# Optimization experiments

Measured on AMD Instinct MI355X. Metric: run time of the kernel, lower is better.

The kernel has to match this reference:

```python
import jax, jax.numpy as jnp
import numpy as np

EPS = 1e-7
MAX_NORM = 10.0  # safe_expmap tangent-norm clamp


def _sinh_div(d):
    # sinh(d)/d, stable at d->0
    ds = jnp.maximum(d, 1e-6)
    return jnp.where(d < 1e-6, 1.0, jnp.sinh(ds) / ds)


def _div_sinh(d):
    # d/sinh(d), stable at d->0
    ds = jnp.maximum(d, 1e-6)
    return jnp.where(d < 1e-6, 1.0, ds / jnp.sinh(ds))


def projx(x):
    # re-project onto hyperboloid: x0 = sqrt(1 + ||x_spatial||^2)
    sp = x[..., 1:]
    x0 = jnp.sqrt(1.0 + jnp.sum(sp * sp, -1, keepdims=True))
    return jnp.concatenate([x0, sp], -1)


def logmap0(x):
    # log map at origin o=(1,0,...,0); tangent has first coord 0
    x0 = jnp.clip(x[..., :1], 1.0 + EPS, None)
    d = jnp.arccosh(x0)
    v_sp = _div_sinh(d) * x[..., 1:]
    return jnp.concatenate([jnp.zeros_like(x0), v_sp], -1)


def safe_expmap0(v):
    # exp map at origin with norm clamping for stability
    sp = v[..., 1:]
    n = jnp.sqrt(jnp.sum(sp * sp, -1, keepdims=True))
    scale = jnp.minimum(1.0, MAX_NORM / jnp.maximum(n, EPS))
    sp = sp * scale
    m = jnp.minimum(n, MAX_NORM)
    return jnp.concatenate([jnp.cosh(m), _sinh_div(m) * sp], -1)


def lorentz_inner(x, y):
    return -x[..., :1] * y[..., :1] + jnp.sum(x[..., 1:] * y[..., 1:], -1, keepdims=True)


def logmap(x, y):
    ip = jnp.clip(lorentz_inner(x, y), None, -(1.0 + EPS))
    d = jnp.arccosh(-ip)
    return _div_sinh(d) * (y + ip * x)


def safe_expmap(x, v):
    # exp map at x with Lorentz-norm clamping
    vv = lorentz_inner(v, v)
    n = jnp.sqrt(jnp.clip(vv, 0.0, None))
    scale = jnp.minimum(1.0, MAX_NORM / jnp.maximum(n, EPS))
    v = v * scale
    m = jnp.minimum(n, MAX_NORM)
    return jnp.cosh(m) * x + _sinh_div(m) * v


def lorentz_linear(x_hyp, W, b):
    # Lorentz -> tangent -> linear -> Lorentz
    y_tan = logmap0(x_hyp) @ W.T + b
    return projx(safe_expmap0(y_tan))


def setup_inputs() -> dict:
    key = jax.random.key(0)
    ks = jax.random.split(key, 8)
    N, D, H = 32768, 256, 1024
    z_sp = 0.5 * jax.random.normal(ks[0], (N, D - 1), dtype=jnp.float32)
    z_h = projx(jnp.concatenate([jnp.zeros((N, 1), jnp.float32), z_sp], -1))
    s = lambda fi, fo: (2.0 / (fi + fo)) ** 0.5
    return {
        "z_h": z_h,
        "w0": s(D, H) * jax.random.normal(ks[1], (H, D), dtype=jnp.float32),
        "b0": jnp.zeros((H,), jnp.float32),
        "w1": s(H, H) * jax.random.normal(ks[2], (H, H), dtype=jnp.float32),
        "b1": jnp.zeros((H,), jnp.float32),
        "w2": s(H, D) * jax.random.normal(ks[3], (D, H), dtype=jnp.float32),
        "b2": jnp.zeros((D,), jnp.float32),
        "alpha": jnp.float32(0.7),
        "step_size": jnp.float32(1.0),
    }


def reference(z_h, w0, b0, w1, b1, w2, b2, alpha, step_size):
    # v_tangent branch: x_previous is None, average_velocity is None
    v_tangent = logmap0(z_h)
    v_hyp = projx(safe_expmap0(v_tangent))

    # LorentzMLP (n_layers=2 -> 3 LorentzLinear layers); dropout is identity (eval)
    x = v_hyp
    for W, b in ((w0, b0), (w1, b1)):
        x = lorentz_linear(x, W, b)
        x = projx(safe_expmap0(logmap0(x)))
    v_transformed_hyp = lorentz_linear(x, w2, b2)

    v_transformed = logmap0(v_transformed_hyp)
    step = jax.nn.sigmoid(step_size)
    v_final = step * v_transformed
    z_update = projx(safe_expmap(z_h, v_final))

    a = jax.nn.sigmoid(alpha)
    tangent_direction = logmap(z_h, z_update)
    scaled_tangent = (1.0 - a) * tangent_direction
    z_next = projx(safe_expmap(z_h, scaled_tangent))
    return (z_next, z_h)
```

## Files before the change

### kernel.cpp

```cpp
#include <hip/hip_runtime.h>
#include <math.h>

#define EPSF 1e-7f
#define MAXN 10.0f

typedef unsigned short ushortT;
typedef __bf16 bf16_8 __attribute__((ext_vector_type(8)));
typedef float f32_4 __attribute__((ext_vector_type(4)));

#define MFMA16 __builtin_amdgcn_mfma_f32_16x16x32_bf16
#define BAR asm volatile("s_barrier" ::: "memory")

__device__ __forceinline__ float sinh_div_f(float d) {
    float ds = fmaxf(d, 1e-6f);
    return (d < 1e-6f) ? 1.0f : sinhf(ds) / ds;
}
__device__ __forceinline__ float div_sinh_f(float d) {
    float ds = fmaxf(d, 1e-6f);
    return (d < 1e-6f) ? 1.0f : ds / sinhf(ds);
}
__device__ __forceinline__ float wred(float v) {
#pragma unroll
    for (int off = 32; off > 0; off >>= 1) v += __shfl_xor(v, off, 64);
    return v;
}
__device__ __forceinline__ float red16(float v) {
    v += __shfl_xor(v, 1, 64); v += __shfl_xor(v, 2, 64);
    v += __shfl_xor(v, 4, 64); v += __shfl_xor(v, 8, 64);
    return v;
}
__device__ __forceinline__ void bsplit(float x, ushortT& h, ushortT& l) {
    unsigned u = __float_as_uint(x);
    unsigned r = (u + 0x7fffu + ((u >> 16) & 1u)) >> 16;
    h = (ushortT)r;
    float lo = x - __uint_as_float(r << 16);
    unsigned ul = __float_as_uint(lo);
    l = (ushortT)((ul + 0x7fffu + ((ul >> 16) & 1u)) >> 16);
}
__device__ __forceinline__ void gload_lds16(const void* g, void* l) {
    __builtin_amdgcn_global_load_lds(
        (const __attribute__((address_space(1))) unsigned int*)g,
        (__attribute__((address_space(3))) unsigned int*)l, 16, 0, 0);
}
__device__ __forceinline__ void split_item(const float* __restrict__ x,
                                           ushortT* __restrict__ hi, ushortT* __restrict__ lo,
                                           int idx) {
    float4 v = reinterpret_cast<const float4*>(x)[idx];
    float f[4] = {v.x, v.y, v.z, v.w};
    ushortT hh[4], ll[4];
#pragma unroll
    for (int e = 0; e < 4; ++e) bsplit(f[e], hh[e], ll[e]);
    reinterpret_cast<ushort4*>(hi)[idx] = ushort4{hh[0], hh[1], hh[2], hh[3]};
    reinterpret_cast<ushort4*>(lo)[idx] = ushort4{ll[0], ll[1], ll[2], ll[3]};
}

__global__ void combo1(const float* __restrict__ z, const float* __restrict__ w0,
                       const float* __restrict__ w1,
                       ushortT* __restrict__ p0h, ushortT* __restrict__ p0l,
                       ushortT* __restrict__ w0h, ushortT* __restrict__ w0l,
                       ushortT* __restrict__ w1h, ushortT* __restrict__ w1l, int N) {
    int b = blockIdx.x, tid = threadIdx.x;
    if (b < 256) {
        split_item(w0, w0h, w0l, b * 256 + tid);
        return;
    }
    if (b < 1280) {
        split_item(w1, w1h, w1l, (b - 256) * 256 + tid);
        return;
    }
    int gw = (b - 1280) * 4 + (tid >> 6);
    int lane = tid & 63;
    if (gw >= N) return;
    float4 zv = reinterpret_cast<const float4*>(z + (size_t)gw * 256)[lane];
    float z0 = __shfl(zv.x, 0, 64);
    float x0 = fmaxf(z0, 1.f + EPSF);
    float d = acoshf(x0);
    float f = div_sinh_f(d);
    float vx = (lane == 0) ? 0.f : zv.x * f;
    float vy = zv.y * f, vz = zv.z * f, vw = zv.w * f;
    float ss = wred(vx * vx + vy * vy + vz * vz + vw * vw);
    float n = sqrtf(ss);
    float s = fminf(1.f, MAXN / fmaxf(n, EPSF));
    float o[4] = {vx * s, vy * s, vz * s, vw * s};
    ushortT hh[4], ll[4];
#pragma unroll
    for (int e = 0; e < 4; ++e) bsplit(o[e], hh[e], ll[e]);
    reinterpret_cast<ushort4*>(p0h + (size_t)gw * 256)[lane] = ushort4{hh[0], hh[1], hh[2], hh[3]};
    reinterpret_cast<ushort4*>(p0l + (size_t)gw * 256)[lane] = ushort4{ll[0], ll[1], ll[2], ll[3]};
}

__global__ void rowscale_kernel(const float* __restrict__ partials, float* __restrict__ scale,
                                int N, int nSlices) {
    int r = blockIdx.x * blockDim.x + threadIdx.x;
    if (r >= N) return;
    float s = 0.f;
    for (int k = 0; k < nSlices; ++k) s += partials[(size_t)k * N + r];
    float n = sqrtf(s);
    scale[r] = fminf(1.f, MAXN / fmaxf(n, EPSF));
}

__global__ void combo2(const float* __restrict__ partials, float* __restrict__ s2,
                       const float* __restrict__ w2,
                       ushortT* __restrict__ w2h, ushortT* __restrict__ w2l, int N) {
    int b = blockIdx.x, tid = threadIdx.x;
    if (b < 128) {
        int r = b * 256 + tid;
        if (r >= N) return;
        float s = 0.f;
        for (int k = 0; k < 16; ++k) s += partials[(size_t)k * N + r];
        float n = sqrtf(s);
        s2[r] = fminf(1.f, MAXN / fmaxf(n, EPSF));
        return;
    }
    split_item(w2, w2h, w2l, (b - 128) * 256 + tid);
}

template<int OUTMODE, int IM>
__global__ __launch_bounds__(512, 2) void gemm_v9(
    const ushortT* __restrict__ Ah_g, const ushortT* __restrict__ Al_g,
    const ushortT* __restrict__ Wh_g, const ushortT* __restrict__ Wl_g,
    const float* __restrict__ bias, const float* __restrict__ scaleA,
    float* __restrict__ outF, ushortT* __restrict__ outH, ushortT* __restrict__ outL,
    float* __restrict__ partials, int K, int M, int nColBlk, int Nrows,
    const float* __restrict__ z_g, const float* __restrict__ alpha_p,
    const float* __restrict__ step_p)
{
    constexpr int BM = IM * 32;
    constexpr int AS = BM * 32;
    constexpr int BS = 256 * 32;
    constexpr int BUF = 2 * AS + 2 * BS;
    constexpr int HM = IM / 2;
    __shared__ __align__(16) ushortT lds[2 * BUF];

    const int tid = threadIdx.x;
    const int wid = tid >> 6, lane = tid & 63;
    const int nwg = gridDim.x;
    const int swz = ((int)blockIdx.x & 7) * (nwg >> 3) + ((int)blockIdx.x >> 3);
    const int rb = swz / nColBlk, cb = swz % nColBlk;
    const int rowBase = rb * BM, colBase = cb * 256;

    const int rl = tid >> 2;
    const int ks = (tid & 3) ^ ((rl >> 1) & 3);
    const int d8 = tid * 8;
    const ushortT* gAh0 = Ah_g + (size_t)(rowBase + rl) * K + ks * 8;
    const ushortT* gAl0 = Al_g + (size_t)(rowBase + rl) * K + ks * 8;
    const ushortT* gAh1 = Ah_g + (size_t)(rowBase + 128 + rl) * K + ks * 8;
    const ushortT* gAl1 = Al_g + (size_t)(rowBase + 128 + rl) * K + ks * 8;
    const ushortT* gBh0 = Wh_g + (size_t)(colBase + rl) * K + ks * 8;
    const ushortT* gBh1 = Wh_g + (size_t)(colBase + 128 + rl) * K + ks * 8;
    const ushortT* gBl0 = Wl_g + (size_t)(colBase + rl) * K + ks * 8;
    const ushortT* gBl1 = Wl_g + (size_t)(colBase + 128 + rl) * K + ks * 8;
#define STG(p, dst, nbo, nk) gload_lds16((p) + (nk), &lds[(nbo) + (dst) + d8])

    const int warpM = wid >> 2, warpN = wid & 3;
    const int frow = lane & 15, fk = lane >> 4;
    const int pslot8 = (fk ^ ((frow >> 1) & 3)) * 8;
    const int aoff = (warpM * (IM * 16) + frow) * 32 + pslot8;
    const int boff = (warpN * 64 + frow) * 32 + pslot8;

    f32_4 acc[IM][4];
#pragma unroll
    for (int i = 0; i < IM; ++i)
#pragma unroll
        for (int j = 0; j < 4; ++j) acc[i][j] = f32_4{0.f, 0.f, 0.f, 0.f};

    STG(gAh0, 0, 0, 0);
    if constexpr (IM == 8) STG(gAh1, 4096, 0, 0);
    STG(gAl0, AS, 0, 0);
    if constexpr (IM == 8) STG(gAl1, AS + 4096, 0, 0);
    STG(gBh0, 2 * AS, 0, 0); STG(gBh1, 2 * AS + 4096, 0, 0);
    STG(gBl0, 2 * AS + BS, 0, 0); STG(gBl1, 2 * AS + BS + 4096, 0, 0);
    asm volatile("s_waitcnt vmcnt(0)" ::: "memory");
    BAR;

    const int nt = K >> 5;
    for (int t = 0; t < nt; ++t) {
        const ushortT* lb = &lds[(t & 1) * BUF];
        const int nbo = ((t & 1) ^ 1) * BUF;
        const int nk = (t + 1) << 5;
        const bool more = (t + 1) < nt;

        if (more) {
            STG(gAh0, 0, nbo, nk);
            if constexpr (IM == 8) STG(gAh1, 4096, nbo, nk);
            STG(gAl0, AS, nbo, nk);
            if constexpr (IM == 8) STG(gAl1, AS + 4096, nbo, nk);
            STG(gBh0, 2 * AS, nbo, nk); STG(gBh1, 2 * AS + 4096, nbo, nk);
            STG(gBl0, 2 * AS + BS, nbo, nk); STG(gBl1, 2 * AS + BS + 4096, nbo, nk);
        }

        bf16_8 ah[IM], bh[4], bl[4], al[IM];
#pragma unroll
        for (int i = 0; i < IM; ++i) ah[i] = *reinterpret_cast<const bf16_8*>(&lb[aoff + i * 512]);
#pragma unroll
        for (int j = 0; j < 4; ++j) bh[j] = *reinterpret_cast<const bf16_8*>(&lb[2 * AS + boff + j * 512]);
        __builtin_amdgcn_s_setprio(1);
#pragma unroll
        for (int i = 0; i < IM; ++i)
#pragma unroll
            for (int j = 0; j < 4; ++j) acc[i][j] = MFMA16(ah[i], bh[j], acc[i][j], 0, 0, 0);
        __builtin_amdgcn_s_setprio(0);

#pragma unroll
        for (int j = 0; j < 4; ++j) bl[j] = *reinterpret_cast<const bf16_8*>(&lb[2 * AS + BS + boff + j * 512]);
        __builtin_amdgcn_s_setprio(1);
#pragma unroll
        for (int i = 0; i < IM; ++i)
#pragma unroll
            for (int j = 0; j < 4; ++j) acc[i][j] = MFMA16(ah[i], bl[j], acc[i][j], 0, 0, 0);
        __builtin_amdgcn_s_setprio(0);

#pragma unroll
        for (int i = 0; i < IM; ++i) al[i] = *reinterpret_cast<const bf16_8*>(&lb[AS + aoff + i * 512]);
        __builtin_amdgcn_s_setprio(1);
#pragma unroll
        for (int i = 0; i < IM; ++i)
#pragma unroll
            for (int j = 0; j < 4; ++j) acc[i][j] = MFMA16(al[i], bh[j], acc[i][j], 0, 0, 0);
        __builtin_amdgcn_s_setprio(0);

        asm volatile("s_waitcnt vmcnt(0)" ::: "memory");
        BAR;
    }
#undef STG

    const int cbase = colBase + warpN * 64 + frow;
    if constexpr (OUTMODE == 0) {
        float bv[4];
#pragma unroll
        for (int j = 0; j < 4; ++j) bv[j] = bias[cbase + j * 16];
        const size_t slice = (size_t)(cb * 4 + warpN) * Nrows;
#pragma unroll
        for (int i = 0; i < IM; ++i) {
            const int row0 = rowBase + warpM * (IM * 16) + i * 16 + fk * 4;
            float4 sa4 = float4{1.f, 1.f, 1.f, 1.f};
            if (scaleA) sa4 = *reinterpret_cast<const float4*>(&scaleA[row0]);
            float psum[4];
#pragma unroll
            for (int r = 0; r < 4; ++r) {
                const float sa = reinterpret_cast<const float*>(&sa4)[r];
                const int row = row0 + r;
                const size_t base = (size_t)row * M;
                float ssv = 0.f;
#pragma unroll
                for (int j = 0; j < 4; ++j) {
                    float y = sa * acc[i][j][r] + bv[j];
                    if (j == 0 && cbase == 0) y = 0.f;
                    ushortT h, l;
                    bsplit(y, h, l);
                    outH[base + cbase + j * 16] = h;
                    outL[base + cbase + j * 16] = l;
                    ssv += y * y;
                }
                psum[r] = red16(ssv);
            }
            if (frow == 0) {
#pragma unroll
                for (int r = 0; r < 4; ++r) partials[slice + row0 + r] = psum[r];
            }
        }
    }
    if constexpr (OUTMODE == 2) {
        float* red  = (float*)&lds[0];
        float* bufZ = red;
        float* bufA = red + 128;
        float* bufB = red + 640;
        float* bufC = red + 1664;
        float* bufD = red + 2176;
        const float stepv = 1.f / (1.f + expf(-step_p[0]));
        const float av    = 1.f / (1.f + expf(-alpha_p[0]));
        const int cb0 = warpN * 64 + frow;
        const bool c0own = (cb0 == 0);
        float bv[4];
#pragma unroll
        for (int j = 0; j < 4; ++j) bv[j] = bias[cb0 + j * 16];
        BAR;
#pragma unroll
        for (int ig = 0; ig < 2; ++ig) {
            float yv[2][4][4], zz[2][4][4], z0[2][4], st0[2][4];
#pragma unroll
            for (int ii = 0; ii < 2; ++ii) {
                const int i = ig * 2 + ii;
                const int row0 = warpM * 64 + i * 16 + fk * 4;
                float4 sa4 = float4{1.f, 1.f, 1.f, 1.f};
                if (scaleA) sa4 = *reinterpret_cast<const float4*>(&scaleA[rowBase + row0]);
#pragma unroll
                for (int rr = 0; rr < 4; ++rr) {
                    const float sa = reinterpret_cast<const float*>(&sa4)[rr];
                    const size_t gz = (size_t)(rowBase + row0 + rr) * 256 + cb0;
#pragma unroll
                    for (int j = 0; j < 4; ++j) {
                        yv[ii][j][rr] = sa * acc[i][j][rr] + bv[j];
                        zz[ii][j][rr] = z_g[gz + j * 16];
                    }
                }
            }
#pragma unroll
            for (int ii = 0; ii < 2; ++ii) {
                const int row0 = warpM * 64 + (ig * 2 + ii) * 16 + fk * 4;
#pragma unroll
                for (int rr = 0; rr < 4; ++rr) {
                    float p = 0.f;
#pragma unroll
                    for (int j = 0; j < 4; ++j) {
                        float yq = (c0own && j == 0) ? 0.f : yv[ii][j][rr];
                        p += yq * yq;
                    }
                    p = red16(p);
                    if (frow == 0) bufA[(row0 + rr) * 4 + warpN] = p;
                    if (c0own) bufZ[row0 + rr] = zz[ii][0][rr];
                }
            }
            BAR;
#pragma unroll
            for (int ii = 0; ii < 2; ++ii) {
                const int row0 = warpM * 64 + (ig * 2 + ii) * 16 + fk * 4;
#pragma unroll
                for (int rr = 0; rr < 4; ++rr) {
                    const int rw = row0 + rr;
                    float ss2 = bufA[rw * 4] + bufA[rw * 4 + 1] + bufA[rw * 4 + 2] + bufA[rw * 4 + 3];
                    z0[ii][rr] = bufZ[rw];
                    float n2 = sqrtf(ss2);
                    float k1 = fminf(1.f, MAXN / fmaxf(n2, EPSF)) * stepv;
                    float n  = k1 * n2;
                    float scv = fminf(1.f, MAXN / fmaxf(n, EPSF));
                    float m  = fminf(n, MAXN);
                    float ch = coshf(m), sdv = sinh_div_f(m);
                    float pe = 0.f, pz = 0.f;
#pragma unroll
                    for (int j = 0; j < 4; ++j) {
                        float vf = (c0own && j == 0) ? 0.f : yv[ii][j][rr] * k1;
                        float e  = ch * zz[ii][j][rr] + sdv * scv * vf;
                        yv[ii][j][rr] = e;
                        if (!(c0own && j == 0)) { pe += e * e; pz += zz[ii][j][rr] * e; }
                    }
                    pe = red16(pe); pz = red16(pz);
                    if (frow == 0) { bufB[rw * 8 + warpN * 2] = pe; bufB[rw * 8 + warpN * 2 + 1] = pz; }
                }
            }
            BAR;
#pragma unroll
            for (int ii = 0; ii < 2; ++ii) {
                const int row0 = warpM * 64 + (ig * 2 + ii) * 16 + fk * 4;
#pragma unroll
                for (int rr = 0; rr < 4; ++rr) {
                    const int rw = row0 + rr;
                    float r3 = bufB[rw * 8] + bufB[rw * 8 + 2] + bufB[rw * 8 + 4] + bufB[rw * 8 + 6];
                    float r4 = bufB[rw * 8 + 1] + bufB[rw * 8 + 3] + bufB[rw * 8 + 5] + bufB[rw * 8 + 7];
                    float u0 = sqrtf(1.f + r3);
                    float ip = fminf(r4 - z0[ii][rr] * u0, -(1.f + EPSF));
                    float dd = acoshf(-ip);
                    float g = div_sinh_f(dd);
                    float oa = (1.f - av) * g;
                    st0[ii][rr] = oa * (u0 + ip * z0[ii][rr]);
                    float p5 = 0.f;
#pragma unroll
                    for (int j = 0; j < 4; ++j) {
                        float st = oa * (yv[ii][j][rr] + ip * zz[ii][j][rr]);
                        yv[ii][j][rr] = st;
                        if (!(c0own && j == 0)) p5 += st * st;
                    }
                    p5 = red16(p5);
                    if (frow == 0) bufC[rw * 4 + warpN] = p5;
                }
            }
            BAR;
#pragma unroll
            for (int ii = 0; ii < 2; ++ii) {
                const int row0 = warpM * 64 + (ig * 2 + ii) * 16 + fk * 4;
#pragma unroll
                for (int rr = 0; rr < 4; ++rr) {
                    const int rw = row0 + rr;
                    float r5 = bufC[rw * 4] + bufC[rw * 4 + 1] + bufC[rw * 4 + 2] + bufC[rw * 4 + 3];
                    float vv2 = r5 - st0[ii][rr] * st0[ii][rr];
                    float n5 = sqrtf(fmaxf(vv2, 0.f));
                    float s5 = fminf(1.f, MAXN / fmaxf(n5, EPSF));
                    float m5 = fminf(n5, MAXN);
                    float ch5 = coshf(m5), sd5 = sinh_div_f(m5);
                    float p6 = 0.f;
#pragma unroll
                    for (int j = 0; j < 4; ++j) {
                        float f = ch5 * zz[ii][j][rr] + sd5 * s5 * yv[ii][j][rr];
                        yv[ii][j][rr] = f;
                        if (!(c0own && j == 0)) p6 += f * f;
                    }
                    p6 = red16(p6);
                    if (frow == 0) bufD[rw * 4 + warpN] = p6;
                }
            }
            BAR;
#pragma unroll
            for (int ii = 0; ii < 2; ++ii) {
                const int row0 = warpM * 64 + (ig * 2 + ii) * 16 + fk * 4;
#pragma unroll
                for (int rr = 0; rr < 4; ++rr) {
                    const int rw = row0 + rr;
                    float r6 = bufD[rw * 4] + bufD[rw * 4 + 1] + bufD[rw * 4 + 2] + bufD[rw * 4 + 3];
                    float zn0 = sqrtf(1.f + r6);
                    const size_t rowG = (size_t)(rowBase + rw);
#pragma unroll
                    for (int j = 0; j < 4; ++j) {
                        const int col = cb0 + j * 16;
                        float v = (c0own && j == 0) ? zn0 : yv[ii][j][rr];
                        outF[rowG * 256 + col] = v;
                        outF[((size_t)Nrows + rowG) * 256 + col] = zz[ii][j][rr];
                    }
                }
            }
        }
    }
}

extern "C" void kernel_launch(void* const* d_in, const int* in_sizes, int n_in,
                              void* d_out, int out_size, void* d_ws, size_t ws_size,
                              hipStream_t stream) {
    const float* z_h  = (const float*)d_in[0];
    const float* w0   = (const float*)d_in[1];
    const float* b0   = (const float*)d_in[2];
    const float* w1   = (const float*)d_in[3];
    const float* b1   = (const float*)d_in[4];
    const float* w2   = (const float*)d_in[5];
    const float* b2   = (const float*)d_in[6];
    const float* alph = (const float*)d_in[7];
    const float* stps = (const float*)d_in[8];
    float* out = (float*)d_out;

    const int D = 256, H = 1024;
    const int N = in_sizes[0] / D;

    char* ob = (char*)d_out;
    ushortT* p0h = (ushortT*)ob;
    ushortT* p0l = (ushortT*)(ob + 16777216);
    char* s2b = ob + 33554432;
    ushortT* w0h = (ushortT*)(s2b);
    ushortT* w0l = (ushortT*)(s2b + 524288);
    ushortT* w1h = (ushortT*)(s2b + 1048576);
    ushortT* w1l = (ushortT*)(s2b + 3145728);
    float* partials = (float*)(s2b + 5242880);
    float* s1 = (float*)(s2b + 7340032);

    ushortT* paH = (ushortT*)d_ws;
    ushortT* paL = paH + (size_t)N * H;
    ushortT* pbH = paL + (size_t)N * H;
    ushortT* pbL = pbH + (size_t)N * H;
    ushortT* w2h = (ushortT*)d_ws;
    ushortT* w2l = (ushortT*)((char*)d_ws + 524288);
    float* s2 = (float*)((char*)d_ws + 1048576);

    combo1<<<1280 + N / 4, 256, 0, stream>>>(z_h, w0, w1, p0h, p0l, w0h, w0l, w1h, w1l, N);

    gemm_v9<0, 8><<<(N / 256) * (H / 256), 512, 0, stream>>>(
        p0h, p0l, w0h, w0l, b0, nullptr, nullptr, paH, paL, partials, D, H, H / 256, N,
        nullptr, nullptr, nullptr);
    rowscale_kernel<<<(N + 255) / 256, 256, 0, stream>>>(partials, s1, N, 16);

    gemm_v9<0, 8><<<(N / 256) * (H / 256), 512, 0, stream>>>(
        paH, paL, w1h, w1l, b1, s1, nullptr, pbH, pbL, partials, H, H, H / 256, N,
        nullptr, nullptr, nullptr);

    combo2<<<384, 256, 0, stream>>>(partials, s2, w2, w2h, w2l, N);

    gemm_v9<2, 4><<<(N / 128) * (D / 256), 512, 0, stream>>>(
        pbH, pbL, w2h, w2l, b2, s2, out, nullptr, nullptr, nullptr, H, D, D / 256, N,
        z_h, alph, stps);
}
```

Measured before the change: 394.8 us.

## Replace 256x256 GEMM tiles with 128x128 interleaved-load kernel for hidden layers

Adds a new gemm_s kernel using 128x128 tiles with 4 warps. It interleaves the global-to-LDS stage loads for the next K-step between the MFMA groups, using partial vmcnt waits and extra barriers rather than issuing all loads up front. The first two Lorentz layers switch to this kernel, and gemm_v9 is trimmed to the IM=4 final-layer path. Smaller tiles quadruple the grid and may improve occupancy and memory/compute overlap, at the cost of more redundant operand loads and more barriers per K-step.

```diff
diff --git a/kernel.cpp b/kernel.cpp
--- a/kernel.cpp
+++ b/kernel.cpp
@@ -115,6 +115,175 @@
     split_item(w2, w2h, w2l, (b - 128) * 256 + tid);
 }
 
+__global__ __launch_bounds__(256, 2) void gemm_s(
+    const ushortT* __restrict__ Ah_g, const ushortT* __restrict__ Al_g,
+    const ushortT* __restrict__ Wh_g, const ushortT* __restrict__ Wl_g,
+    const float* __restrict__ bias, const float* __restrict__ scaleA,
+    ushortT* __restrict__ outH, ushortT* __restrict__ outL,
+    float* __restrict__ partials, int K, int M, int nColBlk, int Nrows)
+{
+    constexpr int AS = 128 * 32;
+    constexpr int BS = 128 * 32;
+    constexpr int BUF = 2 * AS + 2 * BS;
+    __shared__ __align__(16) ushortT lds[2 * BUF];
+
+    const int tid = threadIdx.x;
+    const int wid = tid >> 6, lane = tid & 63;
+    const int nwg = gridDim.x;
+    const int swz = ((int)blockIdx.x & 7) * (nwg >> 3) + ((int)blockIdx.x >> 3);
+    const int rb = swz / nColBlk, cb = swz % nColBlk;
+    const int rowBase = rb * 128, colBase = cb * 128;
+
+    const int rl = tid >> 2;
+    const int ks = (tid & 3) ^ ((rl >> 1) & 3);
+    const int d8 = tid * 8;
+    const ushortT* gAh0 = Ah_g + (size_t)(rowBase + rl) * K + ks * 8;
+    const ushortT* gAh1 = Ah_g + (size_t)(rowBase + 64 + rl) * K + ks * 8;
+    const ushortT* gAl0 = Al_g + (size_t)(rowBase + rl) * K + ks * 8;
+    const ushortT* gAl1 = Al_g + (size_t)(rowBase + 64 + rl) * K + ks * 8;
+    const ushortT* gBh0 = Wh_g + (size_t)(colBase + rl) * K + ks * 8;
+    const ushortT* gBh1 = Wh_g + (size_t)(colBase + 64 + rl) * K + ks * 8;
+    const ushortT* gBl0 = Wl_g + (size_t)(colBase + rl) * K + ks * 8;
+    const ushortT* gBl1 = Wl_g + (size_t)(colBase + 64 + rl) * K + ks * 8;
+#define STG(p, dst, nbo, nk) gload_lds16((p) + (nk), &lds[(nbo) + (dst) + d8])
+
+    const int warpM = wid >> 1, warpN = wid & 1;
+    const int frow = lane & 15, fk = lane >> 4;
+    const int pslot8 = (fk ^ ((frow >> 1) & 3)) * 8;
+    const int aoff = (warpM * 64 + frow) * 32 + pslot8;
+    const int boff = (warpN * 64 + frow) * 32 + pslot8;
+
+    f32_4 acc[4][4];
+#pragma unroll
+    for (int i = 0; i < 4; ++i)
+#pragma unroll
+        for (int j = 0; j < 4; ++j) acc[i][j] = f32_4{0.f, 0.f, 0.f, 0.f};
+
+    STG(gAh0, 0, 0, 0); STG(gAh1, 2048, 0, 0);
+    STG(gAl0, AS, 0, 0); STG(gAl1, AS + 2048, 0, 0);
+    STG(gBh0, 2 * AS, 0, 0); STG(gBh1, 2 * AS + 2048, 0, 0);
+    STG(gBl0, 2 * AS + BS, 0, 0); STG(gBl1, 2 * AS + BS + 2048, 0, 0);
+    asm volatile("s_waitcnt vmcnt(0)" ::: "memory");
+    BAR;
+
+    const int nt = K >> 5;
+    for (int t = 0; t < nt; ++t) {
+        const ushortT* lb = &lds[(t & 1) * BUF];
+        const int nbo = ((t & 1) ^ 1) * BUF;
+        const int nk = (t + 1) << 5;
+        const bool more = (t + 1) < nt;
+        bf16_8 ah[4], bh[4], bl[4], alx[2];
+
+#pragma unroll
+        for (int i = 0; i < 2; ++i) ah[i] = *reinterpret_cast<const bf16_8*>(&lb[aoff + i * 512]);
+#pragma unroll
+        for (int j = 0; j < 4; ++j) bh[j] = *reinterpret_cast<const bf16_8*>(&lb[2 * AS + boff + j * 512]);
+        if (more) { STG(gAh0, 0, nbo, nk); STG(gAh1, 2048, nbo, nk); }
+        BAR;
+        __builtin_amdgcn_s_setprio(1);
+#pragma unroll
+        for (int i = 0; i < 2; ++i)
+#pragma unroll
+            for (int j = 0; j < 4; ++j) acc[i][j] = MFMA16(ah[i], bh[j], acc[i][j], 0, 0, 0);
+        __builtin_amdgcn_s_setprio(0);
+
+#pragma unroll
+        for (int i = 2; i < 4; ++i) ah[i] = *reinterpret_cast<const bf16_8*>(&lb[aoff + i * 512]);
+        if (more) {
+            STG(gAl0, AS, nbo, nk); STG(gAl1, AS + 2048, nbo, nk);
+            asm volatile("s_waitcnt vmcnt(4)" ::: "memory");
+        } else {
+            asm volatile("s_waitcnt vmcnt(0)" ::: "memory");
+        }
+        BAR;
+        __builtin_amdgcn_s_setprio(1);
+#pragma unroll
+        for (int i = 2; i < 4; ++i)
+#pragma unroll
+            for (int j = 0; j < 4; ++j) acc[i][j] = MFMA16(ah[i], bh[j], acc[i][j], 0, 0, 0);
+        __builtin_amdgcn_s_setprio(0);
+
+#pragma unroll
+        for (int j = 0; j < 4; ++j) bl[j] = *reinterpret_cast<const bf16_8*>(&lb[2 * AS + BS + boff + j * 512]);
+        if (more) { STG(gBh0, 2 * AS, nbo, nk); STG(gBh1, 2 * AS + 2048, nbo, nk); }
+        BAR;
+        __builtin_amdgcn_s_setprio(1);
+#pragma unroll
+        for (int i = 0; i < 2; ++i)
+#pragma unroll
+            for (int j = 0; j < 4; ++j) acc[i][j] = MFMA16(ah[i], bl[j], acc[i][j], 0, 0, 0);
+        __builtin_amdgcn_s_setprio(0);
+
+        if (more) { STG(gBl0, 2 * AS + BS, nbo, nk); STG(gBl1, 2 * AS + BS + 2048, nbo, nk); }
+        BAR;
+        __builtin_amdgcn_s_setprio(1);
+#pragma unroll
+        for (int i = 2; i < 4; ++i)
+#pragma unroll
+            for (int j = 0; j < 4; ++j) acc[i][j] = MFMA16(ah[i], bl[j], acc[i][j], 0, 0, 0);
+        __builtin_amdgcn_s_setprio(0);
+
+#pragma unroll
+        for (int i = 0; i < 2; ++i) alx[i] = *reinterpret_cast<const bf16_8*>(&lb[AS + aoff + i * 512]);
+        BAR;
+        __builtin_amdgcn_s_setprio(1);
+#pragma unroll
+        for (int i = 0; i < 2; ++i)
+#pragma unroll
+            for (int j = 0; j < 4; ++j) acc[i][j] = MFMA16(alx[i], bh[j], acc[i][j], 0, 0, 0);
+        __builtin_amdgcn_s_setprio(0);
+
+#pragma unroll
+        for (int i = 0; i < 2; ++i) alx[i] = *reinterpret_cast<const bf16_8*>(&lb[AS + aoff + (2 + i) * 512]);
+        BAR;
+        __builtin_amdgcn_s_setprio(1);
+#pragma unroll
+        for (int i = 0; i < 2; ++i)
+#pragma unroll
+            for (int j = 0; j < 4; ++j) acc[2 + i][j] = MFMA16(alx[i], bh[j], acc[2 + i][j], 0, 0, 0);
+        __builtin_amdgcn_s_setprio(0);
+
+        asm volatile("s_waitcnt vmcnt(2)" ::: "memory");
+        BAR;
+    }
+#undef STG
+
+    const int cbase = colBase + warpN * 64 + frow;
+    float bv[4];
+#pragma unroll
+    for (int j = 0; j < 4; ++j) bv[j] = bias[cbase + j * 16];
+    const size_t slice = (size_t)(cb * 2 + warpN) * Nrows;
+#pragma unroll
+    for (int i = 0; i < 4; ++i) {
+        const int row0 = rowBase + warpM * 64 + i * 16 + fk * 4;
+        float4 sa4 = float4{1.f, 1.f, 1.f, 1.f};
+        if (scaleA) sa4 = *reinterpret_cast<const float4*>(&scaleA[row0]);
+        float psum[4];
+#pragma unroll
+        for (int r = 0; r < 4; ++r) {
+            const float sa = reinterpret_cast<const float*>(&sa4)[r];
+            const int row = row0 + r;
+            const size_t base = (size_t)row * M;
+            float ssv = 0.f;
+#pragma unroll
+            for (int j = 0; j < 4; ++j) {
+                float y = sa * acc[i][j][r] + bv[j];
+                if (j == 0 && cbase == 0) y = 0.f;
+                ushortT h, l;
+                bsplit(y, h, l);
+                outH[base + cbase + j * 16] = h;
+                outL[base + cbase + j * 16] = l;
+                ssv += y * y;
+            }
+            psum[r] = red16(ssv);
+        }
+        if (frow == 0) {
+#pragma unroll
+            for (int r = 0; r < 4; ++r) partials[slice + row0 + r] = psum[r];
+        }
+    }
+}
+
 template<int OUTMODE, int IM>
 __global__ __launch_bounds__(512, 2) void gemm_v9(
     const ushortT* __restrict__ Ah_g, const ushortT* __restrict__ Al_g,
@@ -129,7 +298,6 @@
     constexpr int AS = BM * 32;
     constexpr int BS = 256 * 32;
     constexpr int BUF = 2 * AS + 2 * BS;
-    constexpr int HM = IM / 2;
     __shared__ __align__(16) ushortT lds[2 * BUF];
 
     const int tid = threadIdx.x;
@@ -144,8 +312,6 @@
     const int d8 = tid * 8;
     const ushortT* gAh0 = Ah_g + (size_t)(rowBase + rl) * K + ks * 8;
     const ushortT* gAl0 = Al_g + (size_t)(rowBase + rl) * K + ks * 8;
-    const ushortT* gAh1 = Ah_g + (size_t)(rowBase + 128 + rl) * K + ks * 8;
-    const ushortT* gAl1 = Al_g + (size_t)(rowBase + 128 + rl) * K + ks * 8;
     const ushortT* gBh0 = Wh_g + (size_t)(colBase + rl) * K + ks * 8;
     const ushortT* gBh1 = Wh_g + (size_t)(colBase + 128 + rl) * K + ks * 8;
     const ushortT* gBl0 = Wl_g + (size_t)(colBase + rl) * K + ks * 8;
@@ -165,9 +331,7 @@
         for (int j = 0; j < 4; ++j) acc[i][j] = f32_4{0.f, 0.f, 0.f, 0.f};
 
     STG(gAh0, 0, 0, 0);
-    if constexpr (IM == 8) STG(gAh1, 4096, 0, 0);
     STG(gAl0, AS, 0, 0);
-    if constexpr (IM == 8) STG(gAl1, AS + 4096, 0, 0);
     STG(gBh0, 2 * AS, 0, 0); STG(gBh1, 2 * AS + 4096, 0, 0);
     STG(gBl0, 2 * AS + BS, 0, 0); STG(gBl1, 2 * AS + BS + 4096, 0, 0);
     asm volatile("s_waitcnt vmcnt(0)" ::: "memory");
@@ -182,9 +346,7 @@
 
         if (more) {
             STG(gAh0, 0, nbo, nk);
-            if constexpr (IM == 8) STG(gAh1, 4096, nbo, nk);
             STG(gAl0, AS, nbo, nk);
-            if constexpr (IM == 8) STG(gAl1, AS + 4096, nbo, nk);
             STG(gBh0, 2 * AS, nbo, nk); STG(gBh1, 2 * AS + 4096, nbo, nk);
             STG(gBl0, 2 * AS + BS, nbo, nk); STG(gBl1, 2 * AS + BS + 4096, nbo, nk);
         }
@@ -224,42 +386,6 @@
     }
 #undef STG
 
-    const int cbase = colBase + warpN * 64 + frow;
-    if constexpr (OUTMODE == 0) {
-        float bv[4];
-#pragma unroll
-        for (int j = 0; j < 4; ++j) bv[j] = bias[cbase + j * 16];
-        const size_t slice = (size_t)(cb * 4 + warpN) * Nrows;
-#pragma unroll
-        for (int i = 0; i < IM; ++i) {
-            const int row0 = rowBase + warpM * (IM * 16) + i * 16 + fk * 4;
-            float4 sa4 = float4{1.f, 1.f, 1.f, 1.f};
-            if (scaleA) sa4 = *reinterpret_cast<const float4*>(&scaleA[row0]);
-            float psum[4];
-#pragma unroll
-            for (int r = 0; r < 4; ++r) {
-                const float sa = reinterpret_cast<const float*>(&sa4)[r];
-                const int row = row0 + r;
-                const size_t base = (size_t)row * M;
-                float ssv = 0.f;
-#pragma unroll
-                for (int j = 0; j < 4; ++j) {
-                    float y = sa * acc[i][j][r] + bv[j];
-                    if (j == 0 && cbase == 0) y = 0.f;
-                    ushortT h, l;
-                    bsplit(y, h, l);
-                    outH[base + cbase + j * 16] = h;
-                    outL[base + cbase + j * 16] = l;
-                    ssv += y * y;
-                }
-                psum[r] = red16(ssv);
-            }
-            if (frow == 0) {
-#pragma unroll
-                for (int r = 0; r < 4; ++r) partials[slice + row0 + r] = psum[r];
-            }
-        }
-    }
     if constexpr (OUTMODE == 2) {
         float* red  = (float*)&lds[0];
         float* bufZ = red;
@@ -449,14 +575,12 @@
 
     combo1<<<1280 + N / 4, 256, 0, stream>>>(z_h, w0, w1, p0h, p0l, w0h, w0l, w1h, w1l, N);
 
-    gemm_v9<0, 8><<<(N / 256) * (H / 256), 512, 0, stream>>>(
-        p0h, p0l, w0h, w0l, b0, nullptr, nullptr, paH, paL, partials, D, H, H / 256, N,
-        nullptr, nullptr, nullptr);
+    gemm_s<<<(N / 128) * (H / 128), 256, 0, stream>>>(
+        p0h, p0l, w0h, w0l, b0, nullptr, paH, paL, partials, D, H, H / 128, N);
     rowscale_kernel<<<(N + 255) / 256, 256, 0, stream>>>(partials, s1, N, 16);
 
-    gemm_v9<0, 8><<<(N / 256) * (H / 256), 512, 0, stream>>>(
-        paH, paL, w1h, w1l, b1, s1, nullptr, pbH, pbL, partials, H, H, H / 256, N,
-        nullptr, nullptr, nullptr);
+    gemm_s<<<(N / 128) * (H / 128), 256, 0, stream>>>(
+        paH, paL, w1h, w1l, b1, s1, pbH, pbL, partials, H, H, H / 128, N);
 
     combo2<<<384, 256, 0, stream>>>(partials, s2, w2, w2h, w2l, N);
 
```

Measured after the change: 425.7 us. +7.8%, slower.

## Store low bf16 halves in MFMA-fragment order and load directly from global

Applied to the files above, without the earlier changes.

The low-part bf16 split of activations and weights is now written in a packed layout that matches the per-lane MFMA fragment order. The GEMM then loads these fragments straight from global memory into registers instead of staging them through LDS. This halves LDS traffic and the LDS buffer size per stage, which may improve occupancy or cut LDS pressure. In exchange, producers do scattered 2-byte stores, and the GEMM issues uncached-by-LDS global loads inside the main loop whose latency is not covered by the double buffer.

```diff
diff --git a/kernel.cpp b/kernel.cpp
--- a/kernel.cpp
+++ b/kernel.cpp
@@ -42,16 +42,23 @@
         (const __attribute__((address_space(1))) unsigned int*)g,
         (__attribute__((address_space(3))) unsigned int*)l, 16, 0, 0);
 }
-__device__ __forceinline__ void split_item(const float* __restrict__ x,
-                                           ushortT* __restrict__ hi, ushortT* __restrict__ lo,
-                                           int idx) {
+__device__ __forceinline__ size_t pk(int row, int k, int K) {
+    return (((size_t)(row >> 4) * (size_t)(K >> 5) + (size_t)(k >> 5)) << 9)
+         + (size_t)((((row & 15) + (((k >> 3) & 3) << 4)) << 3) + (k & 7));
+}
+__device__ __forceinline__ void split_item_pk(const float* __restrict__ x,
+                                              ushortT* __restrict__ hi, ushortT* __restrict__ lo,
+                                              int idx, int K) {
     float4 v = reinterpret_cast<const float4*>(x)[idx];
     float f[4] = {v.x, v.y, v.z, v.w};
     ushortT hh[4], ll[4];
 #pragma unroll
     for (int e = 0; e < 4; ++e) bsplit(f[e], hh[e], ll[e]);
     reinterpret_cast<ushort4*>(hi)[idx] = ushort4{hh[0], hh[1], hh[2], hh[3]};
-    reinterpret_cast<ushort4*>(lo)[idx] = ushort4{ll[0], ll[1], ll[2], ll[3]};
+    const int flat = idx * 4;
+    const int row = flat / K, k0 = flat % K;
+#pragma unroll
+    for (int e = 0; e < 4; ++e) lo[pk(row, k0 + e, K)] = ll[e];
 }
 
 __global__ void combo1(const float* __restrict__ z, const float* __restrict__ w0,
@@ -61,11 +68,11 @@
                        ushortT* __restrict__ w1h, ushortT* __restrict__ w1l, int N) {
     int b = blockIdx.x, tid = threadIdx.x;
     if (b < 256) {
-        split_item(w0, w0h, w0l, b * 256 + tid);
+        split_item_pk(w0, w0h, w0l, b * 256 + tid, 256);
         return;
     }
     if (b < 1280) {
-        split_item(w1, w1h, w1l, (b - 256) * 256 + tid);
+        split_item_pk(w1, w1h, w1l, (b - 256) * 256 + tid, 1024);
         return;
     }
     int gw = (b - 1280) * 4 + (tid >> 6);
@@ -86,7 +93,8 @@
 #pragma unroll
     for (int e = 0; e < 4; ++e) bsplit(o[e], hh[e], ll[e]);
     reinterpret_cast<ushort4*>(p0h + (size_t)gw * 256)[lane] = ushort4{hh[0], hh[1], hh[2], hh[3]};
-    reinterpret_cast<ushort4*>(p0l + (size_t)gw * 256)[lane] = ushort4{ll[0], ll[1], ll[2], ll[3]};
+#pragma unroll
+    for (int e = 0; e < 4; ++e) p0l[pk(gw, lane * 4 + e, 256)] = ll[e];
 }
 
 __global__ void rowscale_kernel(const float* __restrict__ partials, float* __restrict__ scale,
@@ -112,13 +120,13 @@
         s2[r] = fminf(1.f, MAXN / fmaxf(n, EPSF));
         return;
     }
-    split_item(w2, w2h, w2l, (b - 128) * 256 + tid);
+    split_item_pk(w2, w2h, w2l, (b - 128) * 256 + tid, 1024);
 }
 
 template<int OUTMODE, int IM>
-__global__ __launch_bounds__(512, 2) void gemm_v9(
-    const ushortT* __restrict__ Ah_g, const ushortT* __restrict__ Al_g,
-    const ushortT* __restrict__ Wh_g, const ushortT* __restrict__ Wl_g,
+__global__ __launch_bounds__(512, 2) void gemm_h(
+    const ushortT* __restrict__ Ah_g, const ushortT* __restrict__ Al_pk,
+    const ushortT* __restrict__ Wh_g, const ushortT* __restrict__ Wl_pk,
     const float* __restrict__ bias, const float* __restrict__ scaleA,
     float* __restrict__ outF, ushortT* __restrict__ outH, ushortT* __restrict__ outL,
     float* __restrict__ partials, int K, int M, int nColBlk, int Nrows,
@@ -126,10 +134,9 @@
     const float* __restrict__ step_p)
 {
     constexpr int BM = IM * 32;
-    constexpr int AS = BM * 32;
-    constexpr int BS = 256 * 32;
-    constexpr int BUF = 2 * AS + 2 * BS;
-    constexpr int HM = IM / 2;
+    constexpr int ASH = BM * 32;
+    constexpr int BSH = 256 * 32;
+    constexpr int BUF = ASH + BSH;
     __shared__ __align__(16) ushortT lds[2 * BUF];
 
     const int tid = threadIdx.x;
@@ -138,18 +145,15 @@
     const int swz = ((int)blockIdx.x & 7) * (nwg >> 3) + ((int)blockIdx.x >> 3);
     const int rb = swz / nColBlk, cb = swz % nColBlk;
     const int rowBase = rb * BM, colBase = cb * 256;
+    const int Kc = K >> 5;
 
     const int rl = tid >> 2;
     const int ks = (tid & 3) ^ ((rl >> 1) & 3);
     const int d8 = tid * 8;
     const ushortT* gAh0 = Ah_g + (size_t)(rowBase + rl) * K + ks * 8;
-    const ushortT* gAl0 = Al_g + (size_t)(rowBase + rl) * K + ks * 8;
     const ushortT* gAh1 = Ah_g + (size_t)(rowBase + 128 + rl) * K + ks * 8;
-    const ushortT* gAl1 = Al_g + (size_t)(rowBase + 128 + rl) * K + ks * 8;
     const ushortT* gBh0 = Wh_g + (size_t)(colBase + rl) * K + ks * 8;
     const ushortT* gBh1 = Wh_g + (size_t)(colBase + 128 + rl) * K + ks * 8;
-    const ushortT* gBl0 = Wl_g + (size_t)(colBase + rl) * K + ks * 8;
-    const ushortT* gBl1 = Wl_g + (size_t)(colBase + 128 + rl) * K + ks * 8;
 #define STG(p, dst, nbo, nk) gload_lds16((p) + (nk), &lds[(nbo) + (dst) + d8])
 
     const int warpM = wid >> 2, warpN = wid & 3;
@@ -158,6 +162,9 @@
     const int aoff = (warpM * (IM * 16) + frow) * 32 + pslot8;
     const int boff = (warpN * 64 + frow) * 32 + pslot8;
 
+    const ushortT* Alp = Al_pk + ((size_t)((rowBase + warpM * IM * 16) >> 4) * Kc << 9) + lane * 8;
+    const ushortT* Blp = Wl_pk + ((size_t)((colBase + warpN * 64) >> 4) * Kc << 9) + lane * 8;
+
     f32_4 acc[IM][4];
 #pragma unroll
     for (int i = 0; i < IM; ++i)
@@ -166,10 +173,7 @@
 
     STG(gAh0, 0, 0, 0);
     if constexpr (IM == 8) STG(gAh1, 4096, 0, 0);
-    STG(gAl0, AS, 0, 0);
-    if constexpr (IM == 8) STG(gAl1, AS + 4096, 0, 0);
-    STG(gBh0, 2 * AS, 0, 0); STG(gBh1, 2 * AS + 4096, 0, 0);
-    STG(gBl0, 2 * AS + BS, 0, 0); STG(gBl1, 2 * AS + BS + 4096, 0, 0);
+    STG(gBh0, ASH, 0, 0); STG(gBh1, ASH + 4096, 0, 0);
     asm volatile("s_waitcnt vmcnt(0)" ::: "memory");
     BAR;
 
@@ -179,39 +183,36 @@
         const int nbo = ((t & 1) ^ 1) * BUF;
         const int nk = (t + 1) << 5;
         const bool more = (t + 1) < nt;
-
+        const size_t t512 = (size_t)t << 9;
+
+        bf16_8 ah[IM], bh[4], bl[4], al[IM];
+#pragma unroll
+        for (int j = 0; j < 4; ++j)
+            bl[j] = *reinterpret_cast<const bf16_8*>(Blp + ((size_t)j * Kc << 9) + t512);
         if (more) {
             STG(gAh0, 0, nbo, nk);
             if constexpr (IM == 8) STG(gAh1, 4096, nbo, nk);
-            STG(gAl0, AS, nbo, nk);
-            if constexpr (IM == 8) STG(gAl1, AS + 4096, nbo, nk);
-            STG(gBh0, 2 * AS, nbo, nk); STG(gBh1, 2 * AS + 4096, nbo, nk);
-            STG(gBl0, 2 * AS + BS, nbo, nk); STG(gBl1, 2 * AS + BS + 4096, nbo, nk);
+            STG(gBh0, ASH, nbo, nk); STG(gBh1, ASH + 4096, nbo, nk);
         }
-
-        bf16_8 ah[IM], bh[4], bl[4], al[IM];
 #pragma unroll
         for (int i = 0; i < IM; ++i) ah[i] = *reinterpret_cast<const bf16_8*>(&lb[aoff + i * 512]);
 #pragma unroll
-        for (int j = 0; j < 4; ++j) bh[j] = *reinterpret_cast<const bf16_8*>(&lb[2 * AS + boff + j * 512]);
+        for (int j = 0; j < 4; ++j) bh[j] = *reinterpret_cast<const bf16_8*>(&lb[ASH + boff + j * 512]);
         __builtin_amdgcn_s_setprio(1);
 #pragma unroll
         for (int i = 0; i < IM; ++i)
 #pragma unroll
             for (int j = 0; j < 4; ++j) acc[i][j] = MFMA16(ah[i], bh[j], acc[i][j], 0, 0, 0);
         __builtin_amdgcn_s_setprio(0);
-
-#pragma unroll
-        for (int j = 0; j < 4; ++j) bl[j] = *reinterpret_cast<const bf16_8*>(&lb[2 * AS + BS + boff + j * 512]);
+#pragma unroll
+        for (int i = 0; i < IM; ++i)
+            al[i] = *reinterpret_cast<const bf16_8*>(Alp + ((size_t)i * Kc << 9) + t512);
         __builtin_amdgcn_s_setprio(1);
 #pragma unroll
         for (int i = 0; i < IM; ++i)
 #pragma unroll
             for (int j = 0; j < 4; ++j) acc[i][j] = MFMA16(ah[i], bl[j], acc[i][j], 0, 0, 0);
         __builtin_amdgcn_s_setprio(0);
-
-#pragma unroll
-        for (int i = 0; i < IM; ++i) al[i] = *reinterpret_cast<const bf16_8*>(&lb[AS + aoff + i * 512]);
         __builtin_amdgcn_s_setprio(1);
 #pragma unroll
         for (int i = 0; i < IM; ++i)
@@ -244,12 +245,13 @@
                 float ssv = 0.f;
 #pragma unroll
                 for (int j = 0; j < 4; ++j) {
+                    const int col = cbase + j * 16;
                     float y = sa * acc[i][j][r] + bv[j];
                     if (j == 0 && cbase == 0) y = 0.f;
                     ushortT h, l;
                     bsplit(y, h, l);
-                    outH[base + cbase + j * 16] = h;
-                    outL[base + cbase + j * 16] = l;
+                    outH[base + col] = h;
+                    outL[pk(row, col, M)] = l;
                     ssv += y * y;
                 }
                 psum[r] = red16(ssv);
@@ -449,18 +451,18 @@
 
     combo1<<<1280 + N / 4, 256, 0, stream>>>(z_h, w0, w1, p0h, p0l, w0h, w0l, w1h, w1l, N);
 
-    gemm_v9<0, 8><<<(N / 256) * (H / 256), 512, 0, stream>>>(
+    gemm_h<0, 8><<<(N / 256) * (H / 256), 512, 0, stream>>>(
         p0h, p0l, w0h, w0l, b0, nullptr, nullptr, paH, paL, partials, D, H, H / 256, N,
         nullptr, nullptr, nullptr);
     rowscale_kernel<<<(N + 255) / 256, 256, 0, stream>>>(partials, s1, N, 16);
 
-    gemm_v9<0, 8><<<(N / 256) * (H / 256), 512, 0, stream>>>(
+    gemm_h<0, 8><<<(N / 256) * (H / 256), 512, 0, stream>>>(
         paH, paL, w1h, w1l, b1, s1, nullptr, pbH, pbL, partials, H, H, H / 256, N,
         nullptr, nullptr, nullptr);
 
     combo2<<<384, 256, 0, stream>>>(partials, s2, w2, w2h, w2l, N);
 
-    gemm_v9<2, 4><<<(N / 128) * (D / 256), 512, 0, stream>>>(
+    gemm_h<2, 4><<<(N / 128) * (D / 256), 512, 0, stream>>>(
         pbH, pbL, w2h, w2l, b2, s2, out, nullptr, nullptr, nullptr, H, D, D / 256, N,
         z_h, alph, stps);
 }
```

New measurement: 431.3 us. 1.09x slower.
